# Kernel optimization log

Hardware: AMD Instinct MI355X
Metric: run time of the kernel (lower is better)

The kernel has to match this reference:

```python
import jax, jax.numpy as jnp
import numpy as np

N_NODES = 100000
N_EDGES = 1600000
IN_DIM = 64
OUT_DIM = 64


def setup_inputs() -> dict:
    key = jax.random.key(0)
    k1, k2, k3, k4, k5, k6 = jax.random.split(key, 6)
    # xavier-uniform-ish scales for the linear weights (gain=1.414)
    fc_bound = 1.414 * np.sqrt(6.0 / (IN_DIM + OUT_DIM))
    at_bound = 1.414 * np.sqrt(6.0 / (OUT_DIM + 1))
    return {
        "h_src": jax.random.normal(k1, (N_NODES, IN_DIM), dtype=jnp.float32),
        "h_dst": jax.random.normal(k2, (N_NODES, IN_DIM), dtype=jnp.float32),
        "W_fc": jax.random.uniform(k3, (OUT_DIM, IN_DIM), dtype=jnp.float32,
                                   minval=-fc_bound, maxval=fc_bound),
        "w_attn": jax.random.uniform(k4, (OUT_DIM,), dtype=jnp.float32,
                                     minval=-at_bound, maxval=at_bound),
        "src": jax.random.randint(k5, (N_EDGES,), 0, N_NODES, dtype=jnp.int64),
        "dst": jnp.sort(jax.random.randint(k6, (N_EDGES,), 0, N_NODES, dtype=jnp.int64)),
    }


def reference(h_src, h_dst, W_fc, w_attn, src, dst):
    # Per-edge feature difference: dst - src  (edge_attention)
    diff_e = h_dst[dst] - h_src[src]                      # [E, in_dim]
    # fc projection (dropout p=0 in eval) then attention score
    d = diff_e @ W_fc.T                                   # [E, out_dim]
    e = jnp.tanh(d @ w_attn)                              # [E]
    # Segment softmax over incoming edges of each destination node
    m = jax.ops.segment_max(e, dst, num_segments=N_NODES)  # [N], -inf for empty
    ex = jnp.exp(e - m[dst])                              # [E]
    s = jax.ops.segment_sum(ex, dst, num_segments=N_NODES)  # [N]
    alpha = ex / s[dst]                                   # [E]
    # Weighted sum aggregation of projected diffs per destination node
    h_diff = jax.ops.segment_sum(alpha[:, None] * d, dst, num_segments=N_NODES)  # [N, out_dim]
    return jax.nn.elu(h_diff)
```

## Files before the change

### kernel.cpp

```cpp
#include <hip/hip_runtime.h>
#include <hip/hip_fp16.h>
#include <math.h>

#define NN 100000
#define NE 1600000
#define DIM 64

__device__ __forceinline__ __half2 u2h2(unsigned u) { __half2 h; __builtin_memcpy(&h, &u, 4); return h; }
__device__ __forceinline__ unsigned h22u(__half2 h) { unsigned u; __builtin_memcpy(&u, &h, 4); return u; }
__device__ __forceinline__ unsigned pk_f16(float a, float b) {
    auto h = __builtin_amdgcn_cvt_pkrtz(a, b);
    unsigned u; __builtin_memcpy(&u, &h, 4); return u;
}

#define WS 68

__global__ __launch_bounds__(256) void proj_kernel(
    const float* __restrict__ h_src, const float* __restrict__ h_dst,
    const float* __restrict__ W, const float* __restrict__ w_attn,
    unsigned* __restrict__ p16, float* __restrict__ a_src, float* __restrict__ a_dst) {
    __shared__ __align__(16) float Wt[DIM * WS];
    __shared__ __align__(16) float Ht[DIM * WS];
    __shared__ __align__(16) float was[DIM];

    const int t = threadIdx.x;
    const int row0 = blockIdx.x * 64;

#pragma unroll
    for (int r = 0; r < 16; ++r) {
        int idx = r * 256 + t;
        int j = idx >> 6, k = idx & 63;
        Wt[k * WS + j] = W[idx];
    }
    if (t < DIM) was[t] = w_attn[t];

    {
        int k = t & 63;
        int nb = t >> 6;
#pragma unroll
        for (int r = 0; r < 16; ++r) {
            int nl = r * 4 + nb;
            int row = row0 + nl;
            const float* hp = (row < NN) ? (h_src + (size_t)row * DIM)
                                         : (h_dst + (size_t)(row - NN) * DIM);
            Ht[k * WS + nl] = hp[k];
        }
    }
    __syncthreads();

    const int jg = (t & 15) * 4;
    const int ng = (t >> 4) * 4;
    float acc[4][4];
#pragma unroll
    for (int a = 0; a < 4; ++a)
#pragma unroll
        for (int b = 0; b < 4; ++b) acc[a][b] = 0.f;

#pragma unroll 4
    for (int k = 0; k < DIM; ++k) {
        const float4 wv = *(const float4*)(Wt + k * WS + jg);
        const float4 hv = *(const float4*)(Ht + k * WS + ng);
        const float wa[4] = {wv.x, wv.y, wv.z, wv.w};
        const float ha[4] = {hv.x, hv.y, hv.z, hv.w};
#pragma unroll
        for (int a = 0; a < 4; ++a)
#pragma unroll
            for (int b = 0; b < 4; ++b) acc[a][b] += ha[a] * wa[b];
    }

    const float4 wat4 = *(const float4*)(was + jg);
#pragma unroll
    for (int a = 0; a < 4; ++a) {
        int row = row0 + ng + a;
        uint2 pk;
        pk.x = pk_f16(acc[a][0], acc[a][1]);
        pk.y = pk_f16(acc[a][2], acc[a][3]);
        *(uint2*)(p16 + (size_t)row * 32 + (jg >> 1)) = pk;

        float pa = acc[a][0] * wat4.x + acc[a][1] * wat4.y +
                   acc[a][2] * wat4.z + acc[a][3] * wat4.w;
#pragma unroll
        for (int off = 8; off; off >>= 1) pa += __shfl_xor(pa, off);
        if ((t & 15) == 0) {
            if (row < NN) a_src[row] = pa;
            else a_dst[row - NN] = pa;
        }
    }
}

__global__ void rowptr_kernel(const int* __restrict__ dst, int* __restrict__ row_ptr) {
    int i = blockIdx.x * blockDim.x + threadIdx.x;
    if (i >= NE) return;
    int d = dst[i];
    int prev = (i == 0) ? -1 : dst[i - 1];
    for (int n = prev + 1; n <= d; ++n) row_ptr[n] = i;
    if (i == NE - 1) {
        for (int n = d + 1; n <= NN; ++n) row_ptr[n] = NE;
    }
}

__global__ __launch_bounds__(256) void agg_kernel(
    const char* __restrict__ p16base,
    const float* __restrict__ a_src, const float* __restrict__ a_dst,
    const int* __restrict__ src, const int* __restrict__ row_ptr,
    float4* __restrict__ out4) {
    __shared__ uint2 buf[4][64];
    const int wv = threadIdx.x >> 6;
    const int lane = threadIdx.x & 63;
    const int g = lane >> 4;
    const int glane = lane & 15;
    const int sub16 = glane >> 3;
    const int chunk = glane & 7;

    const int wid = (blockIdx.x * 4 + wv) * 4 + g;
    if (wid >= NN) return;

    const int beg = row_ptr[wid];
    const int end = row_ptr[wid + 1];
    const bool nonempty = end > beg;

    const float ad = nonempty ? a_dst[wid] : 0.f;
    const char* pbase = p16base + (size_t)chunk * 16;
    uint2* bufw = buf[wv];
    const int gbase = g * 16;

    float sAcc = 0.f;
    __half2 acc[4];
#pragma unroll
    for (int q = 0; q < 4; ++q) acc[q] = u2h2(0u);

    for (int cb = beg; cb < end; cb += 16) {
        int cd = end - cb; if (cd > 16) cd = 16;
        uint2 pk = make_uint2(0u, 0u);
        float w = 0.f;
        if (glane < cd) {
            int sv = src[cb + glane];
            float x = ad - a_src[sv];
            float th = 1.f - 2.f / (__expf(2.f * x) + 1.f);
            w = __expf(th);
            pk.x = pk_f16(w, w);
            pk.y = (unsigned)sv * 128u;
        }
        sAcc += w;
        bufw[lane] = pk;

        for (int j = 0; j < cd; j += 4) {
            uint2 e0 = bufw[gbase + j + sub16];
            uint2 e1 = bufw[gbase + j + 2 + sub16];
            uint4 r0 = *(const uint4*)(pbase + e0.y);
            uint4 r1 = *(const uint4*)(pbase + e1.y);
            __half2 w0 = u2h2(e0.x), w1 = u2h2(e1.x);
            acc[0] = __hfma2(w0, u2h2(r0.x), acc[0]);
            acc[1] = __hfma2(w0, u2h2(r0.y), acc[1]);
            acc[2] = __hfma2(w0, u2h2(r0.z), acc[2]);
            acc[3] = __hfma2(w0, u2h2(r0.w), acc[3]);
            acc[0] = __hfma2(w1, u2h2(r1.x), acc[0]);
            acc[1] = __hfma2(w1, u2h2(r1.y), acc[1]);
            acc[2] = __hfma2(w1, u2h2(r1.z), acc[2]);
            acc[3] = __hfma2(w1, u2h2(r1.w), acc[3]);
        }
    }

#pragma unroll
    for (int off = 1; off <= 8; off <<= 1) sAcc += __shfl_xor(sAcc, off);
#pragma unroll
    for (int q = 0; q < 4; ++q)
        acc[q] = __hadd2(acc[q], u2h2(__shfl_xor(h22u(acc[q]), 8)));

    if (sub16 == 0) {
        const uint4 pdu = *(const uint4*)(p16base + ((size_t)(NN + wid)) * 128 + (size_t)chunk * 16);
        const unsigned pw[4] = {pdu.x, pdu.y, pdu.z, pdu.w};
        const float inv = nonempty ? 1.f / sAcc : 0.f;
        float o[8];
#pragma unroll
        for (int q = 0; q < 4; ++q) {
            float2 pf = __half22float2(u2h2(pw[q]));
            float2 af = __half22float2(acc[q]);
            float h0 = nonempty ? (pf.x - af.x * inv) : 0.f;
            float h1 = nonempty ? (pf.y - af.y * inv) : 0.f;
            o[2 * q]     = h0 > 0.f ? h0 : __expf(h0) - 1.f;
            o[2 * q + 1] = h1 > 0.f ? h1 : __expf(h1) - 1.f;
        }
        const size_t ob = (size_t)wid * 16 + chunk * 2;
        out4[ob]     = make_float4(o[0], o[1], o[2], o[3]);
        out4[ob + 1] = make_float4(o[4], o[5], o[6], o[7]);
    }
}

extern "C" void kernel_launch(void* const* d_in, const int* in_sizes, int n_in,
                              void* d_out, int out_size, void* d_ws, size_t ws_size,
                              hipStream_t stream) {
    const float* h_src = (const float*)d_in[0];
    const float* h_dst = (const float*)d_in[1];
    const float* W     = (const float*)d_in[2];
    const float* w_at  = (const float*)d_in[3];
    const int*   src   = (const int*)d_in[4];
    const int*   dst   = (const int*)d_in[5];

    char* ws = (char*)d_ws;
    unsigned* p16 = (unsigned*)ws;
    float* a_src = (float*)(ws + (size_t)2 * NN * 32 * 4);
    float* a_dst = a_src + NN;
    int* row_ptr = (int*)(a_dst + NN);

    hipLaunchKernelGGL(proj_kernel, dim3((2 * NN) / 64), dim3(256), 0, stream,
                       h_src, h_dst, W, w_at, p16, a_src, a_dst);
    hipLaunchKernelGGL(rowptr_kernel, dim3((NE + 255) / 256), dim3(256), 0, stream,
                       dst, row_ptr);
    hipLaunchKernelGGL(agg_kernel, dim3((NN + 15) / 16), dim3(256), 0, stream,
                       (const char*)p16, a_src, a_dst, src, row_ptr,
                       (float4*)d_out);
}
```

Measured before the change: 164.7 us.

## Use fp16 MFMA for node projection with vectorized loads and staged store

Rewrites the projection GEMM to convert H and W tiles to fp16 in shared memory and compute them with 16x16x32 MFMA instructions instead of scalar FP32 FMAs. Global loads become float4 and the packed fp16 output is staged through LDS for coalesced 16-byte stores. Rounding the inputs to fp16 before the matmul lowers precision compared with the FP32 accumulate, and the attention scalar is still computed from the FP32 MFMA accumulators. Only the projection kernel changes; aggregation is untouched, so the gain is limited to that stage's share of the runtime.

```diff
diff --git a/kernel.cpp b/kernel.cpp
--- a/kernel.cpp
+++ b/kernel.cpp
@@ -5,6 +5,10 @@
 #define NN 100000
 #define NE 1600000
 #define DIM 64
+#define HST 72
+
+typedef __attribute__((ext_vector_type(8))) __fp16 half8;
+typedef __attribute__((ext_vector_type(4))) float f32x4;
 
 __device__ __forceinline__ __half2 u2h2(unsigned u) { __half2 h; __builtin_memcpy(&h, &u, 4); return h; }
 __device__ __forceinline__ unsigned h22u(__half2 h) { unsigned u; __builtin_memcpy(&u, &h, 4); return u; }
@@ -13,78 +17,95 @@
     unsigned u; __builtin_memcpy(&u, &h, 4); return u;
 }
 
-#define WS 68
-
 __global__ __launch_bounds__(256) void proj_kernel(
     const float* __restrict__ h_src, const float* __restrict__ h_dst,
     const float* __restrict__ W, const float* __restrict__ w_attn,
     unsigned* __restrict__ p16, float* __restrict__ a_src, float* __restrict__ a_dst) {
-    __shared__ __align__(16) float Wt[DIM * WS];
-    __shared__ __align__(16) float Ht[DIM * WS];
-    __shared__ __align__(16) float was[DIM];
+    __shared__ __align__(16) unsigned short Hh[64 * HST];
+    __shared__ __align__(16) unsigned short Wh[64 * HST];
+    __shared__ float was[DIM];
 
     const int t = threadIdx.x;
     const int row0 = blockIdx.x * 64;
 
 #pragma unroll
-    for (int r = 0; r < 16; ++r) {
-        int idx = r * 256 + t;
+    for (int r = 0; r < 4; ++r) {
+        int idx = (r * 256 + t) * 4;
         int j = idx >> 6, k = idx & 63;
-        Wt[k * WS + j] = W[idx];
+        float4 v = *(const float4*)(W + idx);
+        uint2 pk; pk.x = pk_f16(v.x, v.y); pk.y = pk_f16(v.z, v.w);
+        *(uint2*)((char*)Wh + j * (HST * 2) + k * 2) = pk;
     }
     if (t < DIM) was[t] = w_attn[t];
 
-    {
-        int k = t & 63;
-        int nb = t >> 6;
-#pragma unroll
-        for (int r = 0; r < 16; ++r) {
-            int nl = r * 4 + nb;
-            int row = row0 + nl;
-            const float* hp = (row < NN) ? (h_src + (size_t)row * DIM)
-                                         : (h_dst + (size_t)(row - NN) * DIM);
-            Ht[k * WS + nl] = hp[k];
-        }
+#pragma unroll
+    for (int r = 0; r < 4; ++r) {
+        int idx = (r * 256 + t) * 4;
+        int row = idx >> 6, k = idx & 63;
+        int grow = row0 + row;
+        const float* hp = (grow < NN) ? h_src + (size_t)grow * DIM
+                                      : h_dst + (size_t)(grow - NN) * DIM;
+        float4 v = *(const float4*)(hp + k);
+        uint2 pk; pk.x = pk_f16(v.x, v.y); pk.y = pk_f16(v.z, v.w);
+        *(uint2*)((char*)Hh + row * (HST * 2) + k * 2) = pk;
     }
     __syncthreads();
 
-    const int jg = (t & 15) * 4;
-    const int ng = (t >> 4) * 4;
-    float acc[4][4];
-#pragma unroll
-    for (int a = 0; a < 4; ++a)
-#pragma unroll
-        for (int b = 0; b < 4; ++b) acc[a][b] = 0.f;
-
-#pragma unroll 4
-    for (int k = 0; k < DIM; ++k) {
-        const float4 wv = *(const float4*)(Wt + k * WS + jg);
-        const float4 hv = *(const float4*)(Ht + k * WS + ng);
-        const float wa[4] = {wv.x, wv.y, wv.z, wv.w};
-        const float ha[4] = {hv.x, hv.y, hv.z, hv.w};
-#pragma unroll
-        for (int a = 0; a < 4; ++a)
-#pragma unroll
-            for (int b = 0; b < 4; ++b) acc[a][b] += ha[a] * wa[b];
-    }
-
-    const float4 wat4 = *(const float4*)(was + jg);
-#pragma unroll
-    for (int a = 0; a < 4; ++a) {
-        int row = row0 + ng + a;
-        uint2 pk;
-        pk.x = pk_f16(acc[a][0], acc[a][1]);
-        pk.y = pk_f16(acc[a][2], acc[a][3]);
-        *(uint2*)(p16 + (size_t)row * 32 + (jg >> 1)) = pk;
-
-        float pa = acc[a][0] * wat4.x + acc[a][1] * wat4.y +
-                   acc[a][2] * wat4.z + acc[a][3] * wat4.w;
-#pragma unroll
-        for (int off = 8; off; off >>= 1) pa += __shfl_xor(pa, off);
-        if ((t & 15) == 0) {
-            if (row < NN) a_src[row] = pa;
-            else a_dst[row - NN] = pa;
-        }
+    const int wv = t >> 6, lane = t & 63;
+    const int col = lane & 15, quad = lane >> 4;
+    const int m0 = wv * 16;
+
+    const char* Hb = (const char*)Hh + (m0 + col) * (HST * 2) + quad * 16;
+    half8 af0 = *(const half8*)(Hb);
+    half8 af1 = *(const half8*)(Hb + 64);
+
+    f32x4 c[4];
+#pragma unroll
+    for (int n = 0; n < 4; ++n) {
+        const char* Bb = (const char*)Wh + (n * 16 + col) * (HST * 2) + quad * 16;
+        half8 b0 = *(const half8*)(Bb);
+        half8 b1 = *(const half8*)(Bb + 64);
+        f32x4 acc = {0.f, 0.f, 0.f, 0.f};
+        acc = __builtin_amdgcn_mfma_f32_16x16x32_f16(af0, b0, acc, 0, 0, 0);
+        acc = __builtin_amdgcn_mfma_f32_16x16x32_f16(af1, b1, acc, 0, 0, 0);
+        c[n] = acc;
+    }
+
+    float wv4[4];
+#pragma unroll
+    for (int n = 0; n < 4; ++n) wv4[n] = was[n * 16 + col];
+#pragma unroll
+    for (int reg = 0; reg < 4; ++reg) {
+        float pa = c[0][reg] * wv4[0] + c[1][reg] * wv4[1] +
+                   c[2][reg] * wv4[2] + c[3][reg] * wv4[3];
+#pragma unroll
+        for (int off = 1; off <= 8; off <<= 1) pa += __shfl_xor(pa, off);
+        if (col == 0) {
+            int grow = row0 + m0 + quad * 4 + reg;
+            if (grow < NN) a_src[grow] = pa;
+            else a_dst[grow - NN] = pa;
+        }
+    }
+
+    __syncthreads();
+    unsigned* Pd = (unsigned*)Hh;
+#pragma unroll
+    for (int n = 0; n < 4; ++n) {
+#pragma unroll
+        for (int reg = 0; reg < 4; ++reg) {
+            float other = __shfl_xor(c[n][reg], 1);
+            if (!(col & 1)) {
+                unsigned pk = pk_f16(c[n][reg], other);
+                Pd[(m0 + quad * 4 + reg) * 32 + (n * 16 + col) / 2] = pk;
+            }
+        }
+    }
+    __syncthreads();
+#pragma unroll
+    for (int r = 0; r < 2; ++r) {
+        int idx = (r * 256 + t) * 4;
+        uint4 v = *(const uint4*)(Pd + idx);
+        *(uint4*)(p16 + (size_t)row0 * 32 + idx) = v;
     }
 }
 
```

Result: faster. 152.2 us (-7.6%).
